# Performance work log

Measured on AMD Instinct MI355X. Metric: run time of the kernel, lower is better.

The kernel has to match this reference:

```python
import jax, jax.numpy as jnp
import numpy as np

W_SIZE = 7      # number of windows per spatial dim (Wg = Hg)
CLUSTERS = 7    # adaptive-pool output per dim -> 49 centers per window


def _pool_matrix(in_size, out_size):
    # Row-stochastic matrix replicating torch AdaptiveAvgPool2d along one dim.
    P = np.zeros((out_size, in_size), dtype=np.float32)
    for i in range(out_size):
        s = (i * in_size) // out_size
        e = -((-(i + 1) * in_size) // out_size)  # ceil((i+1)*in/out)
        P[i, s:e] = 1.0 / (e - s)
    return jnp.asarray(P)


def _normalize(x, eps=1e-12):
    n = jnp.linalg.norm(x, axis=-1, keepdims=True)
    return x / jnp.maximum(n, eps)


def _forward(x_in, f_w, f_b, v_w, v_b, p_w, p_b, sim_alpha, sim_beta):
    B, C, H, W = x_in.shape
    Wg = Hg = W_SIZE
    w, h = H // Wg, W // Hg
    K = CLUSTERS * CLUSTERS  # 49 centers per window

    # 'b e (Wg w) (Hg h) -> (b Wg Hg) e w h'
    x = x_in.reshape(B, C, Wg, w, Hg, h).transpose(0, 2, 4, 1, 3, 5)
    x = x.reshape(B * Wg * Hg, C, w, h)
    x1, x2 = x[:, : C // 2], x[:, C // 2 :]

    # 1x1 convs f and v: dim//2 -> dim//16
    f = jnp.einsum('oc,bcwh->bowh', f_w, x1) + f_b[None, :, None, None]
    v = jnp.einsum('oc,bcwh->bowh', v_w, x2) + v_b[None, :, None, None]
    c = f.shape[1]

    Pw, Ph = _pool_matrix(w, CLUSTERS), _pool_matrix(h, CLUSTERS)
    # adaptive avg pool to (7,7)
    centers = jnp.einsum('iw,bcwh,jh->bcij', Pw, f, Ph)               # [Bw,c,7,7]
    value_centers = jnp.einsum('iw,bcwh,jh->bcij', Pw, v, Ph)
    value_centers = value_centers.reshape(-1, c, K).transpose(0, 2, 1)  # [Bw,K,c]

    cf = centers.reshape(-1, c, K).transpose(0, 2, 1)   # [Bw,K,c]
    ff = f.reshape(-1, c, w * h).transpose(0, 2, 1)      # [Bw,N,c]
    sim = jax.nn.sigmoid(
        sim_beta + sim_alpha * jnp.einsum('bmc,bnc->bmn', _normalize(cf), _normalize(ff))
    )  # [Bw,K,N]

    # hard assignment: each pixel attends only to its argmax center
    idx = jnp.argmax(sim, axis=1)                                   # [Bw,N]
    mask = (jnp.arange(K)[None, :, None] == idx[:, None, :]).astype(sim.dtype)
    sim = sim * mask

    v2 = v.reshape(-1, c, w * h).transpose(0, 2, 1)                 # [Bw,N,c]
    agg = (jnp.einsum('bmn,bnc->bmc', sim, v2) + value_centers) / (
        jnp.sum(sim, axis=-1, keepdims=True) + 1.0
    )                                                                # [Bw,K,c]
    out = jnp.einsum('bmn,bmc->bnc', sim, agg)                       # [Bw,N,c]

    out = out.transpose(0, 2, 1).reshape(-1, c, w, h)
    # '(b Wg Hg) e w h -> b e (Wg w) (Hg h)'
    out = out.reshape(B, Wg, Hg, c, w, h).transpose(0, 3, 1, 4, 2, 5)
    out = out.reshape(B, c, H, W)

    out = jnp.einsum('oc,bchw->bohw', p_w, out) + p_b[None, :, None, None]
    return out.reshape(B, out.shape[1], H * W)


def setup_inputs():
    key = jax.random.key(0)
    ks = jax.random.split(key, 4)
    B, dim, H, W = 16, 256, 112, 112
    c_in, c_mid = dim // 2, dim // 16
    s_f = 1.0 / np.sqrt(c_in)
    s_p = 1.0 / np.sqrt(c_mid)
    return {
        'x_in': jax.random.normal(ks[0], (B, dim, H, W), jnp.float32),
        'f_w': jax.random.normal(ks[1], (c_mid, c_in), jnp.float32) * s_f,
        'f_b': jnp.zeros((c_mid,), jnp.float32),
        'v_w': jax.random.normal(ks[2], (c_mid, c_in), jnp.float32) * s_f,
        'v_b': jnp.zeros((c_mid,), jnp.float32),
        'p_w': jax.random.normal(ks[3], (dim, c_mid), jnp.float32) * s_p,
        'p_b': jnp.zeros((dim,), jnp.float32),
        'sim_alpha': jnp.ones((1,), jnp.float32),
        'sim_beta': jnp.zeros((1,), jnp.float32),
    }


def reference(x_in, f_w, f_b, v_w, v_b, p_w, p_b, sim_alpha, sim_beta):
    return _forward(x_in, f_w, f_b, v_w, v_b, p_w, p_b, sim_alpha, sim_beta)
```

## Files before the change

### kernel.cpp

```cpp
#include <hip/hip_runtime.h>
#include <math.h>

#define HW 12544
#define IMW 112

__device__ __forceinline__ float np_norm16(const float* a) {
    float q[16];
    #pragma unroll
    for (int i = 0; i < 16; ++i) q[i] = __fmul_rn(a[i], a[i]);
    float r0 = __fadd_rn(q[0], q[8]),  r1 = __fadd_rn(q[1], q[9]);
    float r2 = __fadd_rn(q[2], q[10]), r3 = __fadd_rn(q[3], q[11]);
    float r4 = __fadd_rn(q[4], q[12]), r5 = __fadd_rn(q[5], q[13]);
    float r6 = __fadd_rn(q[6], q[14]), r7 = __fadd_rn(q[7], q[15]);
    float s = __fadd_rn(__fadd_rn(__fadd_rn(r0, r1), __fadd_rn(r2, r3)),
                        __fadd_rn(__fadd_rn(r4, r5), __fadd_rn(r6, r7)));
    return fmaxf(__fsqrt_rn(s), 1e-12f);
}

__global__ __launch_bounds__(256, 3)
void lc_fused(const float* __restrict__ x,
              const float* __restrict__ fw, const float* __restrict__ fb,
              const float* __restrict__ vw, const float* __restrict__ vb,
              const float* __restrict__ pw, const float* __restrict__ pb,
              const float* __restrict__ alpha, const float* __restrict__ beta,
              float* __restrict__ out)
{
    __shared__ __attribute__((aligned(16))) float U[12544];
    __shared__ __attribute__((aligned(16))) float agg_s[784];
    __shared__ __attribute__((aligned(16))) float pb_s[256];

    float* fw_s    = U;
    float* vw_s    = U + 2048;
    float* f_s     = U;
    float* cent_s  = U + 4096;
    float* ncf_s   = U + 4880;
    float* vcent_s = U + 5664;
    float* simsum_s= U + 6448;
    float* Pagg_s  = U;

    const int t  = threadIdx.x;
    const int py = t >> 4, px = t & 15;
    const int b  = blockIdx.x;
    const int batch = b / 49;
    const int rr = b % 49;
    const int gi = rr / 7, gj = rr % 7;
    const int row = gi*16 + py, col = gj*16 + px;

    for (int i = t; i < 2048; i += 256) { fw_s[i] = fw[i]; vw_s[i] = vw[i]; }
    pb_s[t] = pb[t];
    for (int i = t; i < 784; i += 256) { vcent_s[i] = 0.f; agg_s[i] = 0.f; }
    if (t < 49) simsum_s[t] = 0.f;
    __syncthreads();

    const float* xp = x + (size_t)batch*256*HW + row*IMW + col;
    float facc[16], vacc[16];
    #pragma unroll
    for (int o = 0; o < 16; ++o) { facc[o] = 0.f; vacc[o] = vb[o]; }

    for (int c4 = 0; c4 < 32; ++c4) {
        const float* xc = xp + (size_t)(c4*4)*HW;
        float x0 = xc[0], x1 = xc[HW], x2 = xc[2*HW], x3 = xc[3*HW];
        const float* yc = xc + (size_t)128*HW;
        float y0 = yc[0], y1 = yc[HW], y2 = yc[2*HW], y3 = yc[3*HW];
        #pragma unroll
        for (int o = 0; o < 16; ++o) {
            const float* ar = fw_s + o*128 + c4*4;
            float s = facc[o];
            s = __fadd_rn(s, __fmul_rn(ar[0], x0));
            s = __fadd_rn(s, __fmul_rn(ar[1], x1));
            s = __fadd_rn(s, __fmul_rn(ar[2], x2));
            s = __fadd_rn(s, __fmul_rn(ar[3], x3));
            facc[o] = s;
            const float* cr = vw_s + o*128 + c4*4;
            vacc[o] = fmaf(cr[3], y3, fmaf(cr[2], y2, fmaf(cr[1], y1, fmaf(cr[0], y0, vacc[o]))));
        }
    }
    #pragma unroll
    for (int o = 0; o < 16; ++o) facc[o] = __fadd_rn(facc[o], fb[o]);

    __syncthreads();

    {
        float* fr = f_s + t*16;
        #pragma unroll
        for (int o = 0; o < 16; ++o) fr[o] = facc[o];
    }
    {
        const int   wss[7] = {0,2,4,6,9,11,13};
        const int   wee[7] = {3,5,7,10,12,14,16};
        const float wiv[7] = {1.f/3.f,1.f/3.f,1.f/3.f,0.25f,1.f/3.f,1.f/3.f,1.f/3.f};
        for (int i = 0; i < 7; ++i) {
            if (py < wss[i] || py >= wee[i]) continue;
            for (int j = 0; j < 7; ++j) {
                if (px < wss[j] || px >= wee[j]) continue;
                const float sc = wiv[i]*wiv[j];
                float* vb2 = vcent_s + (i*7+j)*16;
                #pragma unroll
                for (int o = 0; o < 16; ++o) atomicAdd(vb2 + o, vacc[o]*sc);
            }
        }
    }
    __syncthreads();

    {
        const int   wss[7] = {0,2,4,6,9,11,13};
        const int   wee[7] = {3,5,7,10,12,14,16};
        const float wiv[7] = {1.f/3.f,1.f/3.f,1.f/3.f,0.25f,1.f/3.f,1.f/3.f,1.f/3.f};
        for (int T = t; T < 784; T += 256) {
            int m = T >> 4, o = T & 15;
            int i = m / 7, j = m % 7;
            float pwv = wiv[i], phv = wiv[j];
            float s = 0.f;
            for (int r = wss[i]; r < wee[i]; ++r)
                for (int cc = wss[j]; cc < wee[j]; ++cc)
                    s = __fadd_rn(s, __fmul_rn(__fmul_rn(pwv, f_s[(r*16 + cc)*16 + o]), phv));
            cent_s[T] = s;
        }
    }
    __syncthreads();

    if (t < 49) {
        float rowv[16];
        #pragma unroll
        for (int o = 0; o < 16; ++o) rowv[o] = cent_s[t*16 + o];
        float n = np_norm16(rowv);
        #pragma unroll
        for (int o = 0; o < 16; ++o) ncf_s[t*16 + o] = __fdiv_rn(rowv[o], n);
    }
    __syncthreads();

    float nff[16];
    {
        float n = np_norm16(facc);
        #pragma unroll
        for (int o = 0; o < 16; ++o) nff[o] = __fdiv_rn(facc[o], n);
    }
    const float al = alpha[0], be = beta[0];
    float best = -1.0f; int bidx = 0;
    for (int m = 0; m < 49; ++m) {
        const float* cm = ncf_s + m*16;
        float s = 0.f;
        #pragma unroll
        for (int o = 0; o < 16; ++o) s = __fadd_rn(s, __fmul_rn(cm[o], nff[o]));
        float z = __fadd_rn(be, __fmul_rn(al, s));
        float sim = __fdiv_rn(1.0f, __fadd_rn(1.0f, expf(-z)));
        if (sim > best) { best = sim; bidx = m; }
    }
    const float simv = best;
    atomicAdd(&simsum_s[bidx], simv);
    {
        float* ab = agg_s + bidx*16;
        #pragma unroll
        for (int o = 0; o < 16; ++o) atomicAdd(ab + o, simv*vacc[o]);
    }
    __syncthreads();

    for (int T = t; T < 784; T += 256) {
        int m = T >> 4;
        agg_s[T] = (agg_s[T] + vcent_s[T]) / (simsum_s[m] + 1.0f);
    }
    __syncthreads();

    {
        const float4* pg = (const float4*)(pw + t*16);
        float4 q0 = pg[0], q1 = pg[1], q2 = pg[2], q3 = pg[3];
        for (int m = 0; m < 49; ++m) {
            const float4* am = (const float4*)(agg_s + m*16);
            float4 a0 = am[0], a1 = am[1], a2 = am[2], a3 = am[3];
            float d;
            d = q0.x*a0.x;
            d = fmaf(q0.y,a0.y,d); d = fmaf(q0.z,a0.z,d); d = fmaf(q0.w,a0.w,d);
            d = fmaf(q1.x,a1.x,d); d = fmaf(q1.y,a1.y,d); d = fmaf(q1.z,a1.z,d);
            d = fmaf(q1.w,a1.w,d); d = fmaf(q2.x,a2.x,d); d = fmaf(q2.y,a2.y,d);
            d = fmaf(q2.z,a2.z,d); d = fmaf(q2.w,a2.w,d); d = fmaf(q3.x,a3.x,d);
            d = fmaf(q3.y,a3.y,d); d = fmaf(q3.z,a3.z,d); d = fmaf(q3.w,a3.w,d);
            Pagg_s[t*49 + m] = d;
        }
    }
    __syncthreads();

    float* op = out + (size_t)batch*256*HW + row*IMW + col;
    #pragma unroll 8
    for (int o = 0; o < 256; ++o) {
        op[(size_t)o*HW] = fmaf(simv, Pagg_s[o*49 + bidx], pb_s[o]);
    }
}

extern "C" void kernel_launch(void* const* d_in, const int* in_sizes, int n_in,
                              void* d_out, int out_size, void* d_ws, size_t ws_size,
                              hipStream_t stream) {
    const float* x  = (const float*)d_in[0];
    const float* fw = (const float*)d_in[1];
    const float* fb = (const float*)d_in[2];
    const float* vw = (const float*)d_in[3];
    const float* vb = (const float*)d_in[4];
    const float* pw = (const float*)d_in[5];
    const float* pb = (const float*)d_in[6];
    const float* al = (const float*)d_in[7];
    const float* be = (const float*)d_in[8];
    float* out = (float*)d_out;

    dim3 grid(784), block(256);
    hipLaunchKernelGGL(lc_fused, grid, block, 0, stream,
                       x, fw, fb, vw, vb, pw, pb, al, be, out);
}
```

Measured before the change: 608.1 us.

## Stage input tiles via global_load_lds, vectorize output stores, shrink LDS

```diff
diff --git a/kernel.cpp b/kernel.cpp
--- a/kernel.cpp
+++ b/kernel.cpp
@@ -3,6 +3,10 @@
 
 #define HW 12544
 #define IMW 112
+
+#define GLOAD_LDS16(gp, lp) __builtin_amdgcn_global_load_lds( \
+    (const __attribute__((address_space(1))) void*)(gp),      \
+    (__attribute__((address_space(3))) void*)(lp), 16, 0, 0)
 
 __device__ __forceinline__ float np_norm16(const float* a) {
     float q[16];
@@ -17,7 +21,7 @@
     return fmaxf(__fsqrt_rn(s), 1e-12f);
 }
 
-__global__ __launch_bounds__(256, 3)
+__global__ __launch_bounds__(256, 4)
 void lc_fused(const float* __restrict__ x,
               const float* __restrict__ fw, const float* __restrict__ fb,
               const float* __restrict__ vw, const float* __restrict__ vb,
@@ -25,12 +29,15 @@
               const float* __restrict__ alpha, const float* __restrict__ beta,
               float* __restrict__ out)
 {
-    __shared__ __attribute__((aligned(16))) float U[12544];
+    __shared__ __attribute__((aligned(16))) float U[8192];
     __shared__ __attribute__((aligned(16))) float agg_s[784];
     __shared__ __attribute__((aligned(16))) float pb_s[256];
+    __shared__ __attribute__((aligned(16))) float simv_s[256];
+    __shared__ __attribute__((aligned(16))) int   bidx_s[256];
 
     float* fw_s    = U;
     float* vw_s    = U + 2048;
+    float* xs      = U + 4096;
     float* f_s     = U;
     float* cent_s  = U + 4096;
     float* ncf_s   = U + 4880;
@@ -38,7 +45,8 @@
     float* simsum_s= U + 6448;
     float* Pagg_s  = U;
 
-    const int t  = threadIdx.x;
+    const int t    = threadIdx.x;
+    const int wave = t >> 6, lane = t & 63;
     const int py = t >> 4, px = t & 15;
     const int b  = blockIdx.x;
     const int batch = b / 49;
@@ -46,38 +54,57 @@
     const int gi = rr / 7, gj = rr % 7;
     const int row = gi*16 + py, col = gj*16 + px;
 
-    for (int i = t; i < 2048; i += 256) { fw_s[i] = fw[i]; vw_s[i] = vw[i]; }
+    for (int i = t; i < 512; i += 256) {
+        ((float4*)fw_s)[i] = ((const float4*)fw)[i];
+        ((float4*)vw_s)[i] = ((const float4*)vw)[i];
+    }
     pb_s[t] = pb[t];
-    for (int i = t; i < 784; i += 256) { vcent_s[i] = 0.f; agg_s[i] = 0.f; }
+    for (int i = t; i < 784; i += 256) agg_s[i] = 0.f;
+
+    const float* xbase = x + (size_t)batch*256*HW
+                       + (size_t)(gi*16 + (lane >> 2))*IMW + gj*16 + (lane & 3)*4;
+
+    float facc[16], vacc[16];
+    #pragma unroll
+    for (int o = 0; o < 16; ++o) { facc[o] = 0.f; vacc[o] = vb[o]; }
+
+    for (int ch = 0; ch < 16; ++ch) {
+        #pragma unroll
+        for (int k = 0; k < 4; ++k) {
+            const int sc = (wave << 2) + k;
+            const int gc = (sc < 8) ? (ch*8 + sc)
+                                    : (120 + ch*8 + sc);
+            GLOAD_LDS16(xbase + (size_t)gc*HW, xs + (sc << 8));
+        }
+        __syncthreads();
+
+        #pragma unroll
+        for (int half = 0; half < 2; ++half) {
+            const int c4 = (ch << 1) + half;
+            const float* xf = xs + ((half*4) << 8) + t;
+            const float* xv = xs + 2048 + ((half*4) << 8) + t;
+            const float x0 = xf[0], x1 = xf[256], x2 = xf[512], x3 = xf[768];
+            const float y0 = xv[0], y1 = xv[256], y2 = xv[512], y3 = xv[768];
+            #pragma unroll
+            for (int o = 0; o < 16; ++o) {
+                const float* ar = fw_s + o*128 + c4*4;
+                float s = facc[o];
+                s = __fadd_rn(s, __fmul_rn(ar[0], x0));
+                s = __fadd_rn(s, __fmul_rn(ar[1], x1));
+                s = __fadd_rn(s, __fmul_rn(ar[2], x2));
+                s = __fadd_rn(s, __fmul_rn(ar[3], x3));
+                facc[o] = s;
+                const float* cr = vw_s + o*128 + c4*4;
+                vacc[o] = fmaf(cr[3], y3, fmaf(cr[2], y2, fmaf(cr[1], y1, fmaf(cr[0], y0, vacc[o]))));
+            }
+        }
+        __syncthreads();
+    }
+    #pragma unroll
+    for (int o = 0; o < 16; ++o) facc[o] = __fadd_rn(facc[o], fb[o]);
+
+    for (int i = t; i < 784; i += 256) vcent_s[i] = 0.f;
     if (t < 49) simsum_s[t] = 0.f;
-    __syncthreads();
-
-    const float* xp = x + (size_t)batch*256*HW + row*IMW + col;
-    float facc[16], vacc[16];
-    #pragma unroll
-    for (int o = 0; o < 16; ++o) { facc[o] = 0.f; vacc[o] = vb[o]; }
-
-    for (int c4 = 0; c4 < 32; ++c4) {
-        const float* xc = xp + (size_t)(c4*4)*HW;
-        float x0 = xc[0], x1 = xc[HW], x2 = xc[2*HW], x3 = xc[3*HW];
-        const float* yc = xc + (size_t)128*HW;
-        float y0 = yc[0], y1 = yc[HW], y2 = yc[2*HW], y3 = yc[3*HW];
-        #pragma unroll
-        for (int o = 0; o < 16; ++o) {
-            const float* ar = fw_s + o*128 + c4*4;
-            float s = facc[o];
-            s = __fadd_rn(s, __fmul_rn(ar[0], x0));
-            s = __fadd_rn(s, __fmul_rn(ar[1], x1));
-            s = __fadd_rn(s, __fmul_rn(ar[2], x2));
-            s = __fadd_rn(s, __fmul_rn(ar[3], x3));
-            facc[o] = s;
-            const float* cr = vw_s + o*128 + c4*4;
-            vacc[o] = fmaf(cr[3], y3, fmaf(cr[2], y2, fmaf(cr[1], y1, fmaf(cr[0], y0, vacc[o]))));
-        }
-    }
-    #pragma unroll
-    for (int o = 0; o < 16; ++o) facc[o] = __fadd_rn(facc[o], fb[o]);
-
     __syncthreads();
 
     {
@@ -147,6 +174,8 @@
         if (sim > best) { best = sim; bidx = m; }
     }
     const float simv = best;
+    simv_s[t] = simv;
+    bidx_s[t] = bidx;
     atomicAdd(&simsum_s[bidx], simv);
     {
         float* ab = agg_s + bidx*16;
@@ -161,28 +190,50 @@
     }
     __syncthreads();
 
-    {
-        const float4* pg = (const float4*)(pw + t*16);
-        float4 q0 = pg[0], q1 = pg[1], q2 = pg[2], q3 = pg[3];
-        for (int m = 0; m < 49; ++m) {
-            const float4* am = (const float4*)(agg_s + m*16);
-            float4 a0 = am[0], a1 = am[1], a2 = am[2], a3 = am[3];
-            float d;
-            d = q0.x*a0.x;
-            d = fmaf(q0.y,a0.y,d); d = fmaf(q0.z,a0.z,d); d = fmaf(q0.w,a0.w,d);
-            d = fmaf(q1.x,a1.x,d); d = fmaf(q1.y,a1.y,d); d = fmaf(q1.z,a1.z,d);
-            d = fmaf(q1.w,a1.w,d); d = fmaf(q2.x,a2.x,d); d = fmaf(q2.y,a2.y,d);
-            d = fmaf(q2.z,a2.z,d); d = fmaf(q2.w,a2.w,d); d = fmaf(q3.x,a3.x,d);
-            d = fmaf(q3.y,a3.y,d); d = fmaf(q3.z,a3.z,d); d = fmaf(q3.w,a3.w,d);
-            Pagg_s[t*49 + m] = d;
-        }
-    }
-    __syncthreads();
-
-    float* op = out + (size_t)batch*256*HW + row*IMW + col;
-    #pragma unroll 8
-    for (int o = 0; o < 256; ++o) {
-        op[(size_t)o*HW] = fmaf(simv, Pagg_s[o*49 + bidx], pb_s[o]);
+    float* out_tile = out + (size_t)batch*256*HW + (size_t)(gi*16)*IMW + gj*16;
+    float* op4 = out_tile + (lane >> 2)*IMW + (lane & 3)*4;
+    const float4 sv4 = *(const float4*)(simv_s + (lane << 2));
+    const int4   bi4 = *(const int4*)  (bidx_s + (lane << 2));
+
+    const int oc6 = t >> 1;
+    const int m0  = (t & 1) ? 25 : 0;
+    const int m1  = (t & 1) ? 49 : 25;
+
+    #pragma unroll
+    for (int half = 0; half < 2; ++half) {
+        {
+            const int o = (half << 7) + oc6;
+            const float4* pg = (const float4*)(pw + o*16);
+            const float4 q0 = pg[0], q1 = pg[1], q2 = pg[2], q3 = pg[3];
+            float* pr = Pagg_s + oc6*49;
+            for (int m = m0; m < m1; ++m) {
+                const float4* am = (const float4*)(agg_s + m*16);
+                float4 a0 = am[0], a1 = am[1], a2 = am[2], a3 = am[3];
+                float d;
+                d = q0.x*a0.x;
+                d = fmaf(q0.y,a0.y,d); d = fmaf(q0.z,a0.z,d); d = fmaf(q0.w,a0.w,d);
+                d = fmaf(q1.x,a1.x,d); d = fmaf(q1.y,a1.y,d); d = fmaf(q1.z,a1.z,d);
+                d = fmaf(q1.w,a1.w,d); d = fmaf(q2.x,a2.x,d); d = fmaf(q2.y,a2.y,d);
+                d = fmaf(q2.z,a2.z,d); d = fmaf(q2.w,a2.w,d); d = fmaf(q3.x,a3.x,d);
+                d = fmaf(q3.y,a3.y,d); d = fmaf(q3.z,a3.z,d); d = fmaf(q3.w,a3.w,d);
+                pr[m] = d;
+            }
+        }
+        __syncthreads();
+        #pragma unroll 8
+        for (int k = 0; k < 32; ++k) {
+            const int oc = (wave << 5) + k;
+            const int o  = (half << 7) + oc;
+            const float* pr = Pagg_s + oc*49;
+            const float pbo = pb_s[o];
+            float4 r;
+            r.x = fmaf(sv4.x, pr[bi4.x], pbo);
+            r.y = fmaf(sv4.y, pr[bi4.y], pbo);
+            r.z = fmaf(sv4.z, pr[bi4.z], pbo);
+            r.w = fmaf(sv4.w, pr[bi4.w], pbo);
+            *(float4*)(op4 + (size_t)o*HW) = r;
+        }
+        __syncthreads();
     }
 }
 
```

New measurement: 550.8 us. -9.4%, faster.
